# Optimization experiments

Hardware: AMD Instinct MI355X
Metric: run time of the kernel (lower is better)

Reference implementation:

```python
import jax, jax.numpy as jnp
import numpy as np

D_MODEL = 512
N_LAYERS = 4
D_STATE = 16
D_CONV = 4
EXPAND = 2
D_INNER = EXPAND * D_MODEL          # 1024
DT_RANK = (D_MODEL + 15) // 16      # 32
BATCH, SEQ = 4, 2048


def setup_inputs() -> dict:
    key = jax.random.key(0)
    ks = jax.random.split(key, 8)
    s = lambda k, shape, scale: jax.random.normal(k, shape, dtype=jnp.float32) * scale
    L = N_LAYERS
    A_init = jnp.log(jnp.arange(1, D_STATE + 1, dtype=jnp.float32))  # mamba S4D-real init
    return {
        "x": s(ks[0], (BATCH, SEQ, D_MODEL), 1.0),
        "norm_w": jnp.ones((L, D_MODEL), jnp.float32),
        "norm_b": jnp.zeros((L, D_MODEL), jnp.float32),
        "in_proj_w": s(ks[1], (L, 2 * D_INNER, D_MODEL), 0.02),
        "conv_w": s(ks[2], (L, D_INNER, D_CONV), 0.2),
        "conv_b": jnp.zeros((L, D_INNER), jnp.float32),
        "x_proj_w": s(ks[3], (L, DT_RANK + 2 * D_STATE, D_INNER), 0.02),
        "dt_proj_w": s(ks[4], (L, D_INNER, DT_RANK), 0.1),
        "dt_proj_b": s(ks[5], (L, D_INNER), 0.1),
        "A_log": jnp.tile(A_init[None, None, :], (L, D_INNER, 1)),
        "D": jnp.ones((L, D_INNER), jnp.float32),
        "out_proj_w": s(ks[6], (L, D_MODEL, D_INNER), 0.02),
    }


def _layernorm(x, w, b):
    mu = x.mean(-1, keepdims=True)
    var = ((x - mu) ** 2).mean(-1, keepdims=True)
    return (x - mu) * jax.lax.rsqrt(var + 1e-5) * w + b


def _causal_conv(x, w, b):
    # x: (B,L,D) depthwise causal conv, width D_CONV
    xT = jnp.pad(x.transpose(0, 2, 1), ((0, 0), (0, 0), (D_CONV - 1, 0)))  # (B,D,L+pad)
    y = jax.lax.conv_general_dilated(
        xT, w[:, None, :], window_strides=(1,), padding='VALID',
        feature_group_count=D_INNER, dimension_numbers=('NCH', 'OIH', 'NCH'))
    return (y + b[None, :, None]).transpose(0, 2, 1)  # (B,L,D)


def _selective_scan(deltaA, deltaBu, C):
    # deltaA, deltaBu: (B,L,D,N); C: (B,L,N) -> y: (B,L,D)
    def step(h, inputs):
        dA, dBu, c = inputs
        h = dA * h + dBu
        return h, jnp.einsum('bdn,bn->bd', h, c)
    h0 = jnp.zeros((deltaA.shape[0], deltaA.shape[2], deltaA.shape[3]), deltaA.dtype)
    _, ys = jax.lax.scan(step, h0, (deltaA.transpose(1, 0, 2, 3),
                                    deltaBu.transpose(1, 0, 2, 3),
                                    C.transpose(1, 0, 2)))
    return ys.transpose(1, 0, 2)


def _mamba_block(x, in_w, cw, cb, xpw, dtw, dtb, A_log, Dp, ow):
    xz = jnp.einsum('bld,ed->ble', x, in_w)            # (B,L,2*D_INNER)
    xi, z = jnp.split(xz, 2, axis=-1)
    u = jax.nn.silu(_causal_conv(xi, cw, cb))          # (B,L,D_INNER)
    xdbl = jnp.einsum('bld,ed->ble', u, xpw)           # (B,L,DT_RANK+2N)
    dt = xdbl[..., :DT_RANK]
    Bm = xdbl[..., DT_RANK:DT_RANK + D_STATE]
    Cm = xdbl[..., DT_RANK + D_STATE:]
    delta = jax.nn.softplus(jnp.einsum('blr,dr->bld', dt, dtw) + dtb)
    A = -jnp.exp(A_log)                                # (D_INNER, N)
    deltaA = jnp.exp(delta[..., None] * A)             # (B,L,D,N)
    deltaBu = delta[..., None] * Bm[:, :, None, :] * u[..., None]
    y = _selective_scan(deltaA, deltaBu, Cm) + u * Dp
    y = y * jax.nn.silu(z)
    return jnp.einsum('bld,od->blo', y, ow)


def reference(x, norm_w, norm_b, in_proj_w, conv_w, conv_b, x_proj_w,
              dt_proj_w, dt_proj_b, A_log, D, out_proj_w):
    for l in range(N_LAYERS):
        res = x
        h = _layernorm(x, norm_w[l], norm_b[l])
        x = _mamba_block(h, in_proj_w[l], conv_w[l], conv_b[l], x_proj_w[l],
                         dt_proj_w[l], dt_proj_b[l], A_log[l], D[l],
                         out_proj_w[l]) + res  # dropout is identity in eval
    return x
```

## Files before the change

### kernel.cpp

```cpp
#include <hip/hip_runtime.h>
#include <math.h>

#define D_MODEL 512
#define N_LAYERS 4
#define D_STATE 16
#define D_CONV 4
#define D_INNER 1024
#define DT_RANK 32
#define BATCH 4
#define SEQ 2048
#define NTOK (BATCH*SEQ)
#define NCHUNK 64
#define CL (SEQ/NCHUNK)
#define LOG2E 1.44269504f

typedef unsigned short ushort_t;
typedef __attribute__((ext_vector_type(8))) short bf8_t;
typedef __attribute__((ext_vector_type(4))) float f4_t;

__device__ __forceinline__ ushort_t f2bf(float f) {
    unsigned u = __float_as_uint(f);
    u += 0x7fffu + ((u >> 16) & 1u);
    return (ushort_t)(u >> 16);
}
__device__ __forceinline__ float bf2f(ushort_t h) {
    return __uint_as_float(((unsigned)h) << 16);
}
__device__ __forceinline__ void gload_lds16(const void* g, void* l) {
    auto* gp = (const __attribute__((address_space(1))) unsigned int*)(unsigned long long)(g);
    auto* lp = (__attribute__((address_space(3))) unsigned int*)(unsigned int)(unsigned long long)(l);
    __builtin_amdgcn_global_load_lds(gp, lp, 16, 0, 0);
}
__device__ __forceinline__ void split4(const float* __restrict__ src,
        ushort_t* __restrict__ dh, ushort_t* __restrict__ dl, int rel)
{
    float4 v = ((const float4*)src)[rel];
    ushort_t h0=f2bf(v.x), h1=f2bf(v.y), h2=f2bf(v.z), h3=f2bf(v.w);
    ((ushort4*)dh)[rel] = make_ushort4(h0,h1,h2,h3);
    ((ushort4*)dl)[rel] = make_ushort4(f2bf(v.x-bf2f(h0)), f2bf(v.y-bf2f(h1)),
                                       f2bf(v.z-bf2f(h2)), f2bf(v.w-bf2f(h3)));
}
__device__ __forceinline__ void mk_dA(float dv, const float* A2, bool geo, float* dA)
{
    if (geo) {
        float r1 = exp2f(dv * A2[0]);
        float r2 = r1*r1, r4 = r2*r2, r8 = r4*r4;
        dA[0]=r1;  dA[1]=r2;     dA[2]=r2*r1;    dA[3]=r4;
        dA[4]=r4*r1; dA[5]=r4*r2; dA[6]=r4*r2*r1; dA[7]=r8;
        dA[8]=r8*r1; dA[9]=r8*r2; dA[10]=r8*r2*r1; dA[11]=r8*r4;
        dA[12]=r8*r4*r1; dA[13]=r8*r4*r2; dA[14]=r8*r4*r2*r1; dA[15]=r8*r8;
    } else {
#pragma unroll
        for (int n = 0; n < 16; ++n) dA[n] = exp2f(dv * A2[n]);
    }
}

__global__ __launch_bounds__(256) void prep(
    const float* __restrict__ x, const float* __restrict__ nw, const float* __restrict__ nb,
    ushort_t* __restrict__ xnh, ushort_t* __restrict__ xnl,
    const float* __restrict__ inw, ushort_t* __restrict__ wih, ushort_t* __restrict__ wil,
    const float* __restrict__ outw, ushort_t* __restrict__ woh, ushort_t* __restrict__ wol,
    const float* __restrict__ xpw, ushort_t* __restrict__ xph, ushort_t* __restrict__ xpl)
{
    int bid = blockIdx.x, tid = threadIdx.x;
    if (bid < 2048) {
        int wave = tid >> 6, lane = tid & 63;
        int row = bid * 4 + wave;
        const float* xr = x + (size_t)row * D_MODEL;
        float v[8];
        float s = 0.f;
#pragma unroll
        for (int i = 0; i < 8; ++i) { v[i] = xr[lane + i*64]; s += v[i]; }
#pragma unroll
        for (int off = 32; off > 0; off >>= 1) s += __shfl_xor(s, off, 64);
        float mu = s * (1.f/512.f);
        float q = 0.f;
#pragma unroll
        for (int i = 0; i < 8; ++i) { float d = v[i]-mu; q += d*d; }
#pragma unroll
        for (int off = 32; off > 0; off >>= 1) q += __shfl_xor(q, off, 64);
        float rstd = rsqrtf(q * (1.f/512.f) + 1e-5f);
#pragma unroll
        for (int i = 0; i < 8; ++i) {
            int e = lane + i*64;
            float vv = (v[i]-mu)*rstd*nw[e] + nb[e];
            ushort_t h = f2bf(vv);
            xnh[(size_t)row*D_MODEL + e] = h;
            xnl[(size_t)row*D_MODEL + e] = f2bf(vv - bf2f(h));
        }
    } else if (bid < 3072) {
        split4(inw, wih, wil, (bid-2048)*256 + tid);
    } else if (bid < 3584) {
        split4(outw, woh, wol, (bid-3072)*256 + tid);
    } else {
        split4(xpw, xph, xpl, (bid-3584)*256 + tid);
    }
}

template<int BM, int BN, bool RES>
__global__ __launch_bounds__(256) void gemm_bf16s(
    const ushort_t* __restrict__ Ahi, const ushort_t* __restrict__ Alo, int lda,
    const ushort_t* __restrict__ Bhi, const ushort_t* __restrict__ Blo, int ldb,
    float* __restrict__ C, int ldc, const float* __restrict__ resid, int K)
{
    constexpr int MR = BM/32, NR = BN/32;
    __shared__ __align__(16) char lds[(2*BM + 2*BN)*64];
    char* lAh = lds;
    char* lAl = lds + BM*64;
    char* lBh = lds + 2*BM*64;
    char* lBl = lds + 2*BM*64 + BN*64;
    int tid = threadIdx.x;
    int lane = tid & 63, wave = tid >> 6;
    int row0 = blockIdx.y * BM, col0 = blockIdx.x * BN;
    int wr = wave >> 1, wc = wave & 1;
    f4_t acc[MR][NR];
#pragma unroll
    for (int m=0;m<MR;++m)
#pragma unroll
        for (int n=0;n<NR;++n)
#pragma unroll
            for (int j=0;j<4;++j) acc[m][n][j] = 0.f;

    int srow = tid >> 2;
    int scol = (tid & 3) * 8;
    int koff = (lane >> 4) * 16;
    int fr = lane & 15;

    for (int k0 = 0; k0 < K; k0 += 32) {
        __syncthreads();
        gload_lds16(Ahi + (size_t)(row0 + srow)*lda + k0 + scol, lAh + wave*1024);
        gload_lds16(Alo + (size_t)(row0 + srow)*lda + k0 + scol, lAl + wave*1024);
        if (BM == 128) {
            gload_lds16(Ahi + (size_t)(row0 + 64 + srow)*lda + k0 + scol, lAh + 4096 + wave*1024);
            gload_lds16(Alo + (size_t)(row0 + 64 + srow)*lda + k0 + scol, lAl + 4096 + wave*1024);
        }
        gload_lds16(Bhi + (size_t)(col0 + srow)*ldb + k0 + scol, lBh + wave*1024);
        gload_lds16(Blo + (size_t)(col0 + srow)*ldb + k0 + scol, lBl + wave*1024);
        if (BN == 128) {
            gload_lds16(Bhi + (size_t)(col0 + 64 + srow)*ldb + k0 + scol, lBh + 4096 + wave*1024);
            gload_lds16(Blo + (size_t)(col0 + 64 + srow)*ldb + k0 + scol, lBl + 4096 + wave*1024);
        }
        __syncthreads();
        bf8_t ah[MR], al[MR], bh[NR], bl[NR];
#pragma unroll
        for (int m=0;m<MR;++m) {
            int r = wr*(BM/2) + m*16 + fr;
            ah[m] = *(const bf8_t*)(lAh + r*64 + koff);
            al[m] = *(const bf8_t*)(lAl + r*64 + koff);
        }
#pragma unroll
        for (int n=0;n<NR;++n) {
            int c = wc*(BN/2) + n*16 + fr;
            bh[n] = *(const bf8_t*)(lBh + c*64 + koff);
            bl[n] = *(const bf8_t*)(lBl + c*64 + koff);
        }
#pragma unroll
        for (int m=0;m<MR;++m)
#pragma unroll
            for (int n=0;n<NR;++n) {
                acc[m][n] = __builtin_amdgcn_mfma_f32_16x16x32_bf16(ah[m], bh[n], acc[m][n], 0,0,0);
                acc[m][n] = __builtin_amdgcn_mfma_f32_16x16x32_bf16(ah[m], bl[n], acc[m][n], 0,0,0);
                acc[m][n] = __builtin_amdgcn_mfma_f32_16x16x32_bf16(al[m], bh[n], acc[m][n], 0,0,0);
            }
    }
    int fq = (lane >> 4) * 4;
#pragma unroll
    for (int m=0;m<MR;++m)
#pragma unroll
        for (int n=0;n<NR;++n)
#pragma unroll
            for (int j=0;j<4;++j) {
                int r = row0 + wr*(BM/2) + m*16 + fq + j;
                int c = col0 + wc*(BN/2) + n*16 + fr;
                float v = acc[m][n][j];
                if (RES) v += resid[(size_t)r*ldc + c];
                C[(size_t)r*ldc + c] = v;
            }
}

__global__ __launch_bounds__(256) void xproj_ks(
    const ushort_t* __restrict__ Ahi, const ushort_t* __restrict__ Alo,
    const ushort_t* __restrict__ Bhi, const ushort_t* __restrict__ Blo,
    float* __restrict__ C)
{
    __shared__ __align__(16) char lds[16384];
    char* lAh = lds;
    char* lAl = lds + 4096;
    char* lBh = lds + 8192;
    char* lBl = lds + 12288;
    int tid = threadIdx.x;
    int lane = tid & 63, wave = tid >> 6;
    int row0 = blockIdx.y * 64;
    int kbeg = blockIdx.x * 256;
    int wr = wave >> 1, wc = wave & 1;
    f4_t acc[2][2];
#pragma unroll
    for (int m=0;m<2;++m)
#pragma unroll
        for (int n=0;n<2;++n)
#pragma unroll
            for (int j=0;j<4;++j) acc[m][n][j] = 0.f;
    int srow = tid >> 2;
    int scol = (tid & 3) * 8;
    int koff = (lane >> 4) * 16;
    int fr = lane & 15;
    for (int k0 = kbeg; k0 < kbeg + 256; k0 += 32) {
        __syncthreads();
        gload_lds16(Ahi + (size_t)(row0 + srow)*D_INNER + k0 + scol, lAh + wave*1024);
        gload_lds16(Alo + (size_t)(row0 + srow)*D_INNER + k0 + scol, lAl + wave*1024);
        gload_lds16(Bhi + (size_t)srow*D_INNER + k0 + scol, lBh + wave*1024);
        gload_lds16(Blo + (size_t)srow*D_INNER + k0 + scol, lBl + wave*1024);
        __syncthreads();
        bf8_t ah[2], al[2], bh[2], bl[2];
#pragma unroll
        for (int m=0;m<2;++m) {
            int r = wr*32 + m*16 + fr;
            ah[m] = *(const bf8_t*)(lAh + r*64 + koff);
            al[m] = *(const bf8_t*)(lAl + r*64 + koff);
        }
#pragma unroll
        for (int n=0;n<2;++n) {
            int c = wc*32 + n*16 + fr;
            bh[n] = *(const bf8_t*)(lBh + c*64 + koff);
            bl[n] = *(const bf8_t*)(lBl + c*64 + koff);
        }
#pragma unroll
        for (int m=0;m<2;++m)
#pragma unroll
            for (int n=0;n<2;++n) {
                acc[m][n] = __builtin_amdgcn_mfma_f32_16x16x32_bf16(ah[m], bh[n], acc[m][n], 0,0,0);
                acc[m][n] = __builtin_amdgcn_mfma_f32_16x16x32_bf16(ah[m], bl[n], acc[m][n], 0,0,0);
                acc[m][n] = __builtin_amdgcn_mfma_f32_16x16x32_bf16(al[m], bh[n], acc[m][n], 0,0,0);
            }
    }
    int fq = (lane >> 4) * 4;
#pragma unroll
    for (int m=0;m<2;++m)
#pragma unroll
        for (int n=0;n<2;++n)
#pragma unroll
            for (int j=0;j<4;++j) {
                int r = row0 + wr*32 + m*16 + fq + j;
                int c = wc*32 + n*16 + fr;
                atomicAdd(&C[(size_t)r*64 + c], acc[m][n][j]);
            }
}

__global__ __launch_bounds__(256) void conv_silu(const float* __restrict__ xz,
                        const float* __restrict__ cw, const float* __restrict__ cb,
                        ushort_t* __restrict__ uh, ushort_t* __restrict__ ul)
{
    int idx = blockIdx.x * 256 + threadIdx.x;
    int d = idx & (D_INNER-1);
    int t = (idx >> 10) & (SEQ-1);
    float w0 = cw[d*4+0], w1 = cw[d*4+1], w2 = cw[d*4+2], w3 = cw[d*4+3];
    float s = cb[d];
    const float* base = xz + ((size_t)(idx >> 10))*2048 + d;
    if (t >= 3) s = fmaf(w0, base[-3*2048], s);
    if (t >= 2) s = fmaf(w1, base[-2*2048], s);
    if (t >= 1) s = fmaf(w2, base[-1*2048], s);
    s = fmaf(w3, base[0], s);
    float uv = s / (1.f + __expf(-s));
    ushort_t h = f2bf(uv);
    uh[idx] = h;
    ul[idx] = f2bf(uv - bf2f(h));
}

__global__ __launch_bounds__(256) void dt_softplus(const float* __restrict__ xdbl,
                        const float* __restrict__ dtw, const float* __restrict__ dtb,
                        float* __restrict__ delta)
{
    __shared__ float xr[8][32];
    int t0 = blockIdx.x * 8;
    int tid = threadIdx.x;
    {
        int tt = tid >> 5, r = tid & 31;
        xr[tt][r] = xdbl[(size_t)(t0+tt)*64 + r];
    }
    __syncthreads();
#pragma unroll
    for (int jj = 0; jj < 4; ++jj) {
        int j = (jj<<8) + tid;
        const float* w = dtw + (size_t)j*DT_RANK;
        float bj = dtb[j];
        float acc[8];
#pragma unroll
        for (int tt=0;tt<8;++tt) acc[tt]=bj;
#pragma unroll
        for (int r=0;r<DT_RANK;r+=4){
            float4 w4 = *(const float4*)(w+r);
#pragma unroll
            for (int tt=0;tt<8;++tt){
                acc[tt] = fmaf(xr[tt][r+0], w4.x, acc[tt]);
                acc[tt] = fmaf(xr[tt][r+1], w4.y, acc[tt]);
                acc[tt] = fmaf(xr[tt][r+2], w4.z, acc[tt]);
                acc[tt] = fmaf(xr[tt][r+3], w4.w, acc[tt]);
            }
        }
#pragma unroll
        for (int tt=0;tt<8;++tt){
            float s = acc[tt];
            float sp = fmaxf(s,0.f) + log1pf(__expf(-fabsf(s)));
            delta[(size_t)(t0+tt)*D_INNER + j] = sp;
        }
    }
}

__global__ __launch_bounds__(256) void scan_partial(const float* __restrict__ delta,
                        const ushort_t* __restrict__ uh, const ushort_t* __restrict__ ul,
                        const float* __restrict__ xdbl,
                        const float* __restrict__ A_log,
                        float* __restrict__ P, float* __restrict__ S)
{
    int d = blockIdx.x * 256 + threadIdx.x;
    int c = blockIdx.y;
    int b = blockIdx.z;
    int t0 = c * CL;
    __shared__ float Bsh[CL][16];
    for (int i = threadIdx.x; i < CL*16; i += 256) {
        int tt = i >> 4, n = i & 15;
        Bsh[tt][n] = xdbl[((size_t)(b*SEQ + t0 + tt))*64 + 32 + n];
    }
    __syncthreads();
    float A2[D_STATE];
#pragma unroll
    for (int n = 0; n < D_STATE; ++n)
        A2[n] = -expf(A_log[(size_t)d*D_STATE + n]) * LOG2E;
    bool geo = true;
#pragma unroll
    for (int n = 1; n < D_STATE; ++n)
        geo = geo && (fabsf(A2[n] - (n+1)*A2[0]) <= 1e-4f*fabsf(A2[n]));
    float h[D_STATE];
#pragma unroll
    for (int n = 0; n < D_STATE; ++n) h[n] = 0.f;
    float sdv = 0.f;
    const float* dl = delta + ((size_t)(b*SEQ + t0))*D_INNER + d;
    const ushort_t* uhp = uh + ((size_t)(b*SEQ + t0))*D_INNER + d;
    const ushort_t* ulp = ul + ((size_t)(b*SEQ + t0))*D_INNER + d;
#pragma unroll 4
    for (int t = 0; t < CL; ++t) {
        float dv = dl[(size_t)t*D_INNER];
        float uv = bf2f(uhp[(size_t)t*D_INNER]) + bf2f(ulp[(size_t)t*D_INNER]);
        float du = dv * uv;
        sdv += dv;
        float dA[D_STATE];
        mk_dA(dv, A2, geo, dA);
#pragma unroll
        for (int n = 0; n < D_STATE; ++n)
            h[n] = fmaf(dA[n], h[n], Bsh[t][n] * du);
    }
    size_t base = (((size_t)b*D_INNER + d)*NCHUNK + c)*16;
#pragma unroll
    for (int n = 0; n < D_STATE; ++n) P[base+n] = exp2f(A2[n]*sdv);
#pragma unroll
    for (int n = 0; n < D_STATE; n += 4)
        *(float4*)&S[base+n] = make_float4(h[n],h[n+1],h[n+2],h[n+3]);
}

__global__ __launch_bounds__(256) void scan_boundary(const float* __restrict__ P,
                        float* __restrict__ S)
{
    int gid = blockIdx.x * 256 + threadIdx.x;
    int n  = gid & 15;
    size_t base = ((size_t)(gid >> 4))*NCHUNK*16 + n;
    float h = 0.f;
    for (int c = 0; c < NCHUNK; ++c) {
        size_t o = base + (size_t)c*16;
        float p = P[o];
        float s = S[o];
        S[o] = h;
        h = fmaf(p, h, s);
    }
}

__global__ __launch_bounds__(256) void scan_final(const float* __restrict__ delta,
                        const ushort_t* __restrict__ uh, const ushort_t* __restrict__ ul,
                        float* __restrict__ xz,
                        const float* __restrict__ xdbl,
                        const float* __restrict__ A_log,
                        const float* __restrict__ Dp,
                        const float* __restrict__ Hs)
{
    int d = blockIdx.x * 256 + threadIdx.x;
    int c = blockIdx.y;
    int b = blockIdx.z;
    int t0 = c * CL;
    __shared__ float Bsh[CL][16];
    __shared__ float Csh[CL][16];
    for (int i = threadIdx.x; i < CL*16; i += 256) {
        int tt = i >> 4, n = i & 15;
        size_t xo = ((size_t)(b*SEQ + t0 + tt))*64;
        Bsh[tt][n] = xdbl[xo + 32 + n];
        Csh[tt][n] = xdbl[xo + 48 + n];
    }
    __syncthreads();
    float A2[D_STATE];
#pragma unroll
    for (int n = 0; n < D_STATE; ++n)
        A2[n] = -expf(A_log[(size_t)d*D_STATE + n]) * LOG2E;
    bool geo = true;
#pragma unroll
    for (int n = 1; n < D_STATE; ++n)
        geo = geo && (fabsf(A2[n] - (n+1)*A2[0]) <= 1e-4f*fabsf(A2[n]));
    float Dd = Dp[d];
    float h[D_STATE];
    size_t hbase = (((size_t)b*D_INNER + d)*NCHUNK + c)*16;
#pragma unroll
    for (int n = 0; n < D_STATE; n += 4) {
        float4 h4 = *(const float4*)&Hs[hbase+n];
        h[n]=h4.x; h[n+1]=h4.y; h[n+2]=h4.z; h[n+3]=h4.w;
    }
    const float* dl = delta + ((size_t)(b*SEQ + t0))*D_INNER + d;
    const ushort_t* uhp = uh + ((size_t)(b*SEQ + t0))*D_INNER + d;
    const ushort_t* ulp = ul + ((size_t)(b*SEQ + t0))*D_INNER + d;
    const float* zl = xz + ((size_t)(b*SEQ + t0))*2048 + 1024 + d;
    ushort_t* yrow = (ushort_t*)(xz + ((size_t)(b*SEQ + t0))*2048);
#pragma unroll 4
    for (int t = 0; t < CL; ++t) {
        float dv = dl[(size_t)t*D_INNER];
        float uv = bf2f(uhp[(size_t)t*D_INNER]) + bf2f(ulp[(size_t)t*D_INNER]);
        float zv = zl[(size_t)t*2048];
        float du = dv * uv;
        float dA[D_STATE];
        mk_dA(dv, A2, geo, dA);
        float y = 0.f;
#pragma unroll
        for (int n = 0; n < D_STATE; ++n) {
            h[n] = fmaf(dA[n], h[n], Bsh[t][n] * du);
            y = fmaf(h[n], Csh[t][n], y);
        }
        y = fmaf(uv, Dd, y);
        float sig = 1.f / (1.f + __expf(-zv));
        float yg = y * (zv * sig);
        ushort_t yh = f2bf(yg);
        yrow[(size_t)t*4096 + d] = yh;
        yrow[(size_t)t*4096 + 1024 + d] = f2bf(yg - bf2f(yh));
    }
}

extern "C" void kernel_launch(void* const* d_in, const int* in_sizes, int n_in,
                              void* d_out, int out_size, void* d_ws, size_t ws_size,
                              hipStream_t stream) {
    const float* x_in   = (const float*)d_in[0];
    const float* norm_w = (const float*)d_in[1];
    const float* norm_b = (const float*)d_in[2];
    const float* in_w   = (const float*)d_in[3];
    const float* conv_w = (const float*)d_in[4];
    const float* conv_b = (const float*)d_in[5];
    const float* xp_w   = (const float*)d_in[6];
    const float* dt_w   = (const float*)d_in[7];
    const float* dt_b   = (const float*)d_in[8];
    const float* A_log  = (const float*)d_in[9];
    const float* Dp     = (const float*)d_in[10];
    const float* out_w  = (const float*)d_in[11];
    float* out = (float*)d_out;

    float* ws   = (float*)d_ws;
    float* xz   = ws;
    ushort_t* uhb = (ushort_t*)(xz + (size_t)NTOK*2048);
    ushort_t* ulb = uhb + (size_t)NTOK*D_INNER;
    float* xdbl = (float*)(ulb + (size_t)NTOK*D_INNER);
    float* dlt  = xdbl + (size_t)NTOK*64;
    float* Pb   = dlt  + (size_t)NTOK*D_INNER;
    float* Sb   = Pb   + (size_t)BATCH*D_INNER*NCHUNK*16;
    ushort_t* wih = (ushort_t*)(Sb + (size_t)BATCH*D_INNER*NCHUNK*16);
    ushort_t* wil = wih + (size_t)2*D_INNER*D_MODEL;
    ushort_t* woh = wil + (size_t)2*D_INNER*D_MODEL;
    ushort_t* wol = woh + (size_t)D_MODEL*D_INNER;
    ushort_t* xph = wol + (size_t)D_MODEL*D_INNER;
    ushort_t* xpl = xph + (size_t)64*D_INNER;
    ushort_t* xnh = (ushort_t*)dlt;
    ushort_t* xnl = xnh + (size_t)NTOK*D_MODEL;

    for (int l = 0; l < N_LAYERS; ++l) {
        const float* xcur = (l == 0) ? x_in : out;
        prep<<<3648, 256, 0, stream>>>(
            xcur, norm_w + l*D_MODEL, norm_b + l*D_MODEL, xnh, xnl,
            in_w + (size_t)l*2*D_INNER*D_MODEL, wih, wil,
            out_w + (size_t)l*D_MODEL*D_INNER, woh, wol,
            xp_w + (size_t)l*64*D_INNER, xph, xpl);
        gemm_bf16s<128,128,false><<<dim3(2048/128, NTOK/128), 256, 0, stream>>>(
            xnh, xnl, D_MODEL, wih, wil, D_MODEL, xz, 2048, nullptr, D_MODEL);
        conv_silu<<<(NTOK*D_INNER)/256, 256, 0, stream>>>(
            xz, conv_w + (size_t)l*D_INNER*D_CONV, conv_b + (size_t)l*D_INNER, uhb, ulb);
        hipMemsetAsync(xdbl, 0, (size_t)NTOK*64*sizeof(float), stream);
        xproj_ks<<<dim3(4, NTOK/64), 256, 0, stream>>>(uhb, ulb, xph, xpl, xdbl);
        dt_softplus<<<NTOK/8, 256, 0, stream>>>(
            xdbl, dt_w + (size_t)l*D_INNER*DT_RANK, dt_b + (size_t)l*D_INNER, dlt);
        scan_partial<<<dim3(D_INNER/256, NCHUNK, BATCH), 256, 0, stream>>>(
            dlt, uhb, ulb, xdbl, A_log + (size_t)l*D_INNER*D_STATE, Pb, Sb);
        scan_boundary<<<256, 256, 0, stream>>>(Pb, Sb);
        scan_final<<<dim3(D_INNER/256, NCHUNK, BATCH), 256, 0, stream>>>(
            dlt, uhb, ulb, xz, xdbl, A_log + (size_t)l*D_INNER*D_STATE, Dp + (size_t)l*D_INNER, Sb);
        gemm_bf16s<64,128,true><<<dim3(D_MODEL/128, NTOK/64), 256, 0, stream>>>(
            (const ushort_t*)xz, (const ushort_t*)xz + 1024, 4096,
            woh, wol, D_INNER, out, D_MODEL, xcur, D_INNER);
    }
}
```

Baseline: 1.254 ms.

## Fuse dt projection and softplus into scan_partial; enlarge out-proj GEMM tile

Removes the separate dt_softplus kernel and computes the delta projection plus softplus inside scan_partial. Each thread keeps its 32 dt weights in registers and reads the dt rows from shared memory, then writes delta for scan_final to use. This saves one launch and the delta read in scan_partial, but adds register pressure and a per-step 32-FMA dot product inside the sequential scan loop. The out-projection GEMM also moves from 64x128 to 128x128 tiles, which halves the block count.

```diff
diff --git a/kernel.cpp b/kernel.cpp
--- a/kernel.cpp
+++ b/kernel.cpp
@@ -266,50 +266,12 @@
     ul[idx] = f2bf(uv - bf2f(h));
 }
 
-__global__ __launch_bounds__(256) void dt_softplus(const float* __restrict__ xdbl,
-                        const float* __restrict__ dtw, const float* __restrict__ dtb,
-                        float* __restrict__ delta)
-{
-    __shared__ float xr[8][32];
-    int t0 = blockIdx.x * 8;
-    int tid = threadIdx.x;
-    {
-        int tt = tid >> 5, r = tid & 31;
-        xr[tt][r] = xdbl[(size_t)(t0+tt)*64 + r];
-    }
-    __syncthreads();
-#pragma unroll
-    for (int jj = 0; jj < 4; ++jj) {
-        int j = (jj<<8) + tid;
-        const float* w = dtw + (size_t)j*DT_RANK;
-        float bj = dtb[j];
-        float acc[8];
-#pragma unroll
-        for (int tt=0;tt<8;++tt) acc[tt]=bj;
-#pragma unroll
-        for (int r=0;r<DT_RANK;r+=4){
-            float4 w4 = *(const float4*)(w+r);
-#pragma unroll
-            for (int tt=0;tt<8;++tt){
-                acc[tt] = fmaf(xr[tt][r+0], w4.x, acc[tt]);
-                acc[tt] = fmaf(xr[tt][r+1], w4.y, acc[tt]);
-                acc[tt] = fmaf(xr[tt][r+2], w4.z, acc[tt]);
-                acc[tt] = fmaf(xr[tt][r+3], w4.w, acc[tt]);
-            }
-        }
-#pragma unroll
-        for (int tt=0;tt<8;++tt){
-            float s = acc[tt];
-            float sp = fmaxf(s,0.f) + log1pf(__expf(-fabsf(s)));
-            delta[(size_t)(t0+tt)*D_INNER + j] = sp;
-        }
-    }
-}
-
-__global__ __launch_bounds__(256) void scan_partial(const float* __restrict__ delta,
+__global__ __launch_bounds__(256) void scan_partial(
                         const ushort_t* __restrict__ uh, const ushort_t* __restrict__ ul,
                         const float* __restrict__ xdbl,
+                        const float* __restrict__ dtw, const float* __restrict__ dtb,
                         const float* __restrict__ A_log,
+                        float* __restrict__ delta,
                         float* __restrict__ P, float* __restrict__ S)
 {
     int d = blockIdx.x * 256 + threadIdx.x;
@@ -317,11 +279,20 @@
     int b = blockIdx.z;
     int t0 = c * CL;
     __shared__ float Bsh[CL][16];
+    __shared__ float dtsh[CL][32];
     for (int i = threadIdx.x; i < CL*16; i += 256) {
         int tt = i >> 4, n = i & 15;
         Bsh[tt][n] = xdbl[((size_t)(b*SEQ + t0 + tt))*64 + 32 + n];
     }
+    for (int i = threadIdx.x; i < CL*32; i += 256) {
+        int tt = i >> 5, r = i & 31;
+        dtsh[tt][r] = xdbl[((size_t)(b*SEQ + t0 + tt))*64 + r];
+    }
     __syncthreads();
+    float wreg[DT_RANK];
+#pragma unroll
+    for (int r = 0; r < DT_RANK; ++r) wreg[r] = dtw[(size_t)d*DT_RANK + r];
+    float bj = dtb[d];
     float A2[D_STATE];
 #pragma unroll
     for (int n = 0; n < D_STATE; ++n)
@@ -334,12 +305,16 @@
 #pragma unroll
     for (int n = 0; n < D_STATE; ++n) h[n] = 0.f;
     float sdv = 0.f;
-    const float* dl = delta + ((size_t)(b*SEQ + t0))*D_INNER + d;
     const ushort_t* uhp = uh + ((size_t)(b*SEQ + t0))*D_INNER + d;
     const ushort_t* ulp = ul + ((size_t)(b*SEQ + t0))*D_INNER + d;
-#pragma unroll 4
+    float* dlp = delta + ((size_t)(b*SEQ + t0))*D_INNER + d;
+#pragma unroll 2
     for (int t = 0; t < CL; ++t) {
-        float dv = dl[(size_t)t*D_INNER];
+        float sraw = bj;
+#pragma unroll
+        for (int r = 0; r < DT_RANK; ++r) sraw = fmaf(dtsh[t][r], wreg[r], sraw);
+        float dv = fmaxf(sraw,0.f) + log1pf(__expf(-fabsf(sraw)));
+        dlp[(size_t)t*D_INNER] = dv;
         float uv = bf2f(uhp[(size_t)t*D_INNER]) + bf2f(ulp[(size_t)t*D_INNER]);
         float du = dv * uv;
         sdv += dv;
@@ -485,14 +460,13 @@
             xz, conv_w + (size_t)l*D_INNER*D_CONV, conv_b + (size_t)l*D_INNER, uhb, ulb);
         hipMemsetAsync(xdbl, 0, (size_t)NTOK*64*sizeof(float), stream);
         xproj_ks<<<dim3(4, NTOK/64), 256, 0, stream>>>(uhb, ulb, xph, xpl, xdbl);
-        dt_softplus<<<NTOK/8, 256, 0, stream>>>(
-            xdbl, dt_w + (size_t)l*D_INNER*DT_RANK, dt_b + (size_t)l*D_INNER, dlt);
         scan_partial<<<dim3(D_INNER/256, NCHUNK, BATCH), 256, 0, stream>>>(
-            dlt, uhb, ulb, xdbl, A_log + (size_t)l*D_INNER*D_STATE, Pb, Sb);
+            uhb, ulb, xdbl, dt_w + (size_t)l*D_INNER*DT_RANK, dt_b + (size_t)l*D_INNER,
+            A_log + (size_t)l*D_INNER*D_STATE, dlt, Pb, Sb);
         scan_boundary<<<256, 256, 0, stream>>>(Pb, Sb);
         scan_final<<<dim3(D_INNER/256, NCHUNK, BATCH), 256, 0, stream>>>(
             dlt, uhb, ulb, xz, xdbl, A_log + (size_t)l*D_INNER*D_STATE, Dp + (size_t)l*D_INNER, Sb);
-        gemm_bf16s<64,128,true><<<dim3(D_MODEL/128, NTOK/64), 256, 0, stream>>>(
+        gemm_bf16s<128,128,true><<<dim3(D_MODEL/128, NTOK/128), 256, 0, stream>>>(
             (const ushort_t*)xz, (const ushort_t*)xz + 1024, 4096,
             woh, wol, D_INNER, out, D_MODEL, xcur, D_INNER);
     }
```

Result: no change. 1.231 ms (-1.8%).
